# Kernel optimization log

Measured on AMD Instinct MI355X. Metric: run time of the kernel, lower is better.

## Reference

```python
import jax, jax.numpy as jnp
import numpy as np

N_NODES = 100000
N_EDGES = 1600000
N_MOVES = 200000
D = 256          # in_channels
H = 512          # hidden_dim

def setup_inputs() -> dict:
    key = jax.random.key(0)
    ks = jax.random.split(key, 6)
    node_embeddings = jax.random.normal(ks[0], (N_NODES, D), dtype=jnp.float32)
    edge_index = jax.random.randint(ks[1], (2, N_EDGES), 0, N_NODES, dtype=jnp.int64)
    move_edge_idxs = jax.random.randint(ks[2], (N_MOVES,), 0, N_EDGES, dtype=jnp.int64)
    # torch Linear weights: [out, in], scaled like kaiming-uniform-ish
    W1 = jax.random.normal(ks[3], (H, 2 * D), dtype=jnp.float32) * (1.0 / np.sqrt(2 * D))
    b1 = jnp.zeros((H,), dtype=jnp.float32)
    W2 = jax.random.normal(ks[4], (H // 2, H), dtype=jnp.float32) * (1.0 / np.sqrt(H))
    b2 = jnp.zeros((H // 2,), dtype=jnp.float32)
    W3 = jax.random.normal(ks[5], (1, H // 2), dtype=jnp.float32) * (1.0 / np.sqrt(H // 2))
    b3 = jnp.zeros((1,), dtype=jnp.float32)
    return {"node_embeddings": node_embeddings, "edge_index": edge_index,
            "move_edge_idxs": move_edge_idxs, "W1": W1, "b1": b1,
            "W2": W2, "b2": b2, "W3": W3, "b3": b3}

def reference(node_embeddings, edge_index, move_edge_idxs, W1, b1, W2, b2, W3, b3):
    # candidate_moves = edge_index[:, move_edge_idxs].T -> [n_moves, 2]
    src = edge_index[0, move_edge_idxs]          # [n_moves]
    tgt = edge_index[1, move_edge_idxs]          # [n_moves]
    emb_src = node_embeddings[src]               # [n_moves, D]
    emb_tgt = node_embeddings[tgt]               # [n_moves, D]
    x = jnp.concatenate([emb_src, emb_tgt], axis=-1)   # [n_moves, 2D]
    # 3-layer MLP (dropout is identity in eval mode)
    h = jax.nn.relu(x @ W1.T + b1)               # [n_moves, H]
    h = jax.nn.relu(h @ W2.T + b2)               # [n_moves, H//2]
    logits = (h @ W3.T + b3).squeeze(-1)         # [n_moves]
    return logits
```

## Files before the change

### kernel.cpp

```cpp
#include <hip/hip_runtime.h>
#include <hip/hip_bf16.h>

typedef __attribute__((ext_vector_type(4))) float f32x4;
typedef __attribute__((ext_vector_type(8))) short bfrag;
typedef __attribute__((ext_vector_type(4))) float facc;
typedef __attribute__((ext_vector_type(8))) ushort u16x8;

#define N_MOVES 200000
#define N_EDGES 1600000
#define DEMB 256
#define KD 512
#define H1D 512
#define H2D 256
#define MT 128
#define NTHREADS 1024

__device__ __forceinline__ ushort f2b(float f) {
  union { float f; unsigned u; } x; x.f = f;
  unsigned r = (x.u + 0x7fffu + ((x.u >> 16) & 1u)) >> 16;
  return (ushort)r;
}
__device__ __forceinline__ float b2f(ushort h) {
  union { unsigned u; float f; } x; x.u = ((unsigned)h) << 16;
  return x.f;
}

__global__ void convert_w(const float* __restrict__ W1, const float* __restrict__ W2,
                          ushort* __restrict__ Wb) {
  int i = (blockIdx.x * 256 + threadIdx.x) * 4;
  const int n1 = H1D * KD;
  if (i < n1) {
    f32x4 v = *(const f32x4*)(W1 + i);
    ushort4 h = { f2b(v.x), f2b(v.y), f2b(v.z), f2b(v.w) };
    *(ushort4*)(Wb + i) = h;
  } else {
    int j = i - n1;
    f32x4 v = *(const f32x4*)(W2 + j);
    ushort4 h = { f2b(v.x), f2b(v.y), f2b(v.z), f2b(v.w) };
    *(ushort4*)(Wb + n1 + j) = h;
  }
}

__global__ void convert_emb(const float* __restrict__ E, ushort* __restrict__ Eb) {
  int i = (blockIdx.x * 256 + threadIdx.x) * 8;
  f32x4 a = *(const f32x4*)(E + i);
  f32x4 b = *(const f32x4*)(E + i + 4);
  u16x8 h = { f2b(a.x), f2b(a.y), f2b(a.z), f2b(a.w),
              f2b(b.x), f2b(b.y), f2b(b.z), f2b(b.w) };
  *(u16x8*)(Eb + i) = h;
}

template<int EMBBF>
__global__ __launch_bounds__(NTHREADS, 4)
void fused_mlp(const float* __restrict__ emb,
               const ushort* __restrict__ embb,
               const int* __restrict__ edge_index,
               const int* __restrict__ move_idx,
               const ushort* __restrict__ W1b,
               const float* __restrict__ b1,
               const ushort* __restrict__ W2b,
               const float* __restrict__ b2,
               const float* __restrict__ W3,
               const float* __restrict__ b3,
               float* __restrict__ out)
{
  __shared__ ushort bufA[MT][KD];
  __shared__ int   s_src[MT], s_tgt[MT];
  __shared__ float sW3[H2D];

  const int tid  = threadIdx.x;
  const int lane = tid & 63;
  const int wave = tid >> 6;
  const int m0   = blockIdx.x * MT;

  if (tid < MT) {
    int mi = m0 + tid;
    if (mi >= N_MOVES) mi = N_MOVES - 1;
    int e = move_idx[mi];
    s_src[tid] = edge_index[e];
    s_tgt[tid] = edge_index[N_EDGES + e];
  }
  if (tid < H2D) sW3[tid] = W3[tid];
  __syncthreads();

  const int arow = lane & 15;
  const int akB  = (lane >> 4) << 4;
  const int nq   = (lane >> 4) << 2;

  const ushort* wp0 = W1b + (size_t)(((wave << 5) + arow) * KD) + (akB >> 1);
  const ushort* wp1 = wp0 + 16 * KD;

  bfrag bA[2], bB[2];
  bA[0] = *(const bfrag*)(wp0);      bA[1] = *(const bfrag*)(wp1);
  bB[0] = *(const bfrag*)(wp0 + 32); bB[1] = *(const bfrag*)(wp1 + 32);

  if (EMBBF) {
    #pragma unroll
    for (int it = 0; it < 8; ++it) {
      int row  = (wave << 3) + it;
      int gl   = lane ^ (row & 7);
      int node = (gl < 32) ? s_src[row] : s_tgt[row];
      const ushort* gp = embb + (size_t)node * DEMB + ((size_t)(gl & 31) << 3);
      __builtin_amdgcn_global_load_lds(
          (const __attribute__((address_space(1))) void*)gp,
          (__attribute__((address_space(3))) void*)(&bufA[row][0]),
          16, 0, 0);
    }
  } else {
    for (int u = tid; u < MT * 128; u += NTHREADS) {
      int row = u >> 7;
      int c4  = u & 127;
      const float* sp = (c4 < 64) ? (emb + (size_t)s_src[row] * DEMB + (c4 << 2))
                                  : (emb + (size_t)s_tgt[row] * DEMB + ((c4 - 64) << 2));
      f32x4 v = *(const f32x4*)sp;
      ushort4 h = { f2b(v.x), f2b(v.y), f2b(v.z), f2b(v.w) };
      int bo = (c4 << 3) ^ ((row & 7) << 4);
      *(ushort4*)((char*)(&bufA[row][0]) + bo) = h;
    }
  }
  __syncthreads();

  facc acc[8][2];
  #pragma unroll
  for (int mg = 0; mg < 8; ++mg) {
    acc[mg][0] = (facc){0.f, 0.f, 0.f, 0.f};
    acc[mg][1] = (facc){0.f, 0.f, 0.f, 0.f};
  }

  bfrag aE[8];
  #pragma unroll
  for (int mg = 0; mg < 8; ++mg) {
    int row = (mg << 4) + arow;
    int bo = akB ^ ((row & 7) << 4);
    aE[mg] = *(const bfrag*)((const char*)(&bufA[row][0]) + bo);
  }

  #pragma unroll
  for (int kk2 = 0; kk2 < 8; ++kk2) {
    const int kk = kk2 << 1;
    __builtin_amdgcn_s_setprio(1);
    #pragma unroll
    for (int mg = 0; mg < 8; ++mg) {
      acc[mg][0] = __builtin_amdgcn_mfma_f32_16x16x32_bf16(bA[0], aE[mg], acc[mg][0], 0, 0, 0);
      acc[mg][1] = __builtin_amdgcn_mfma_f32_16x16x32_bf16(bA[1], aE[mg], acc[mg][1], 0, 0, 0);
    }
    __builtin_amdgcn_s_setprio(0);
    #pragma unroll
    for (int mg = 0; mg < 8; ++mg) {
      int row = (mg << 4) + arow;
      int bo = (((kk + 1) << 6) + akB) ^ ((row & 7) << 4);
      aE[mg] = *(const bfrag*)((const char*)(&bufA[row][0]) + bo);
    }
    if (kk + 2 < 16) {
      bA[0] = *(const bfrag*)(wp0 + ((kk + 2) << 5));
      bA[1] = *(const bfrag*)(wp1 + ((kk + 2) << 5));
    }
    __builtin_amdgcn_s_setprio(1);
    #pragma unroll
    for (int mg = 0; mg < 8; ++mg) {
      acc[mg][0] = __builtin_amdgcn_mfma_f32_16x16x32_bf16(bB[0], aE[mg], acc[mg][0], 0, 0, 0);
      acc[mg][1] = __builtin_amdgcn_mfma_f32_16x16x32_bf16(bB[1], aE[mg], acc[mg][1], 0, 0, 0);
    }
    __builtin_amdgcn_s_setprio(0);
    if (kk2 < 7) {
      #pragma unroll
      for (int mg = 0; mg < 8; ++mg) {
        int row = (mg << 4) + arow;
        int bo = (((kk + 2) << 6) + akB) ^ ((row & 7) << 4);
        aE[mg] = *(const bfrag*)((const char*)(&bufA[row][0]) + bo);
      }
      if (kk + 3 < 16) {
        bB[0] = *(const bfrag*)(wp0 + ((kk + 3) << 5));
        bB[1] = *(const bfrag*)(wp1 + ((kk + 3) << 5));
      }
    }
  }

  const ushort* cp0 = W2b + (size_t)(((wave << 4) + arow) * KD) + (akB >> 1);
  bfrag cA = *(const bfrag*)(cp0);
  bfrag cB = *(const bfrag*)(cp0 + 32);
  f32x4 bv1[2];
  bv1[0] = *(const f32x4*)(b1 + (wave << 5) + nq);
  bv1[1] = *(const f32x4*)(b1 + (wave << 5) + 16 + nq);

  __syncthreads();

  #pragma unroll
  for (int mg = 0; mg < 8; ++mg) {
    int m = (mg << 4) + arow;
    #pragma unroll
    for (int ng = 0; ng < 2; ++ng) {
      int nb = (wave << 5) + (ng << 4) + nq;
      ushort4 h;
      h.x = f2b(fmaxf(acc[mg][ng][0] + bv1[ng][0], 0.f));
      h.y = f2b(fmaxf(acc[mg][ng][1] + bv1[ng][1], 0.f));
      h.z = f2b(fmaxf(acc[mg][ng][2] + bv1[ng][2], 0.f));
      h.w = f2b(fmaxf(acc[mg][ng][3] + bv1[ng][3], 0.f));
      int bo = (nb << 1) ^ ((m & 7) << 4);
      *(ushort4*)((char*)(&bufA[0][0]) + m * (KD * 2) + bo) = h;
    }
  }
  __syncthreads();

  facc acc2[8];
  #pragma unroll
  for (int mg = 0; mg < 8; ++mg) acc2[mg] = (facc){0.f, 0.f, 0.f, 0.f};

  #pragma unroll
  for (int mg = 0; mg < 8; ++mg) {
    int row = (mg << 4) + arow;
    int bo = akB ^ ((row & 7) << 4);
    aE[mg] = *(const bfrag*)((const char*)(&bufA[row][0]) + bo);
  }

  #pragma unroll
  for (int kk2 = 0; kk2 < 8; ++kk2) {
    const int kk = kk2 << 1;
    __builtin_amdgcn_s_setprio(1);
    #pragma unroll
    for (int mg = 0; mg < 8; ++mg)
      acc2[mg] = __builtin_amdgcn_mfma_f32_16x16x32_bf16(cA, aE[mg], acc2[mg], 0, 0, 0);
    __builtin_amdgcn_s_setprio(0);
    #pragma unroll
    for (int mg = 0; mg < 8; ++mg) {
      int row = (mg << 4) + arow;
      int bo = (((kk + 1) << 6) + akB) ^ ((row & 7) << 4);
      aE[mg] = *(const bfrag*)((const char*)(&bufA[row][0]) + bo);
    }
    if (kk + 2 < 16) cA = *(const bfrag*)(cp0 + ((kk + 2) << 5));
    __builtin_amdgcn_s_setprio(1);
    #pragma unroll
    for (int mg = 0; mg < 8; ++mg)
      acc2[mg] = __builtin_amdgcn_mfma_f32_16x16x32_bf16(cB, aE[mg], acc2[mg], 0, 0, 0);
    __builtin_amdgcn_s_setprio(0);
    if (kk2 < 7) {
      #pragma unroll
      for (int mg = 0; mg < 8; ++mg) {
        int row = (mg << 4) + arow;
        int bo = (((kk + 2) << 6) + akB) ^ ((row & 7) << 4);
        aE[mg] = *(const bfrag*)((const char*)(&bufA[row][0]) + bo);
      }
      if (kk + 3 < 16) cB = *(const bfrag*)(cp0 + ((kk + 3) << 5));
    }
  }

  f32x4 bv2 = *(const f32x4*)(b2 + (wave << 4) + nq);

  __syncthreads();

  ushort (*H2s)[H2D] = (ushort(*)[H2D])bufA;
  #pragma unroll
  for (int mg = 0; mg < 8; ++mg) {
    int m = (mg << 4) + arow;
    int nb = (wave << 4) + nq;
    ushort4 h;
    h.x = f2b(fmaxf(acc2[mg][0] + bv2[0], 0.f));
    h.y = f2b(fmaxf(acc2[mg][1] + bv2[1], 0.f));
    h.z = f2b(fmaxf(acc2[mg][2] + bv2[2], 0.f));
    h.w = f2b(fmaxf(acc2[mg][3] + bv2[3], 0.f));
    int bo = (nb << 1) ^ ((m & 7) << 4);
    *(ushort4*)((char*)(&H2s[0][0]) + m * (H2D * 2) + bo) = h;
  }
  __syncthreads();

  {
    const float b3v = b3[0];
    int row = tid >> 3;
    int oct = tid & 7;
    float sum = 0.f;
    #pragma unroll
    for (int j = 0; j < 4; ++j) {
      int kb = (oct << 6) + (j << 4);
      int bo = kb ^ ((row & 7) << 4);
      bfrag hv = *(const bfrag*)((const char*)(&H2s[row][0]) + bo);
      int k0 = (oct << 5) + (j << 3);
      #pragma unroll
      for (int e = 0; e < 8; ++e)
        sum += b2f((ushort)hv[e]) * sW3[k0 + e];
    }
    sum += __shfl_xor(sum, 1);
    sum += __shfl_xor(sum, 2);
    sum += __shfl_xor(sum, 4);
    if (oct == 0 && (m0 + row) < N_MOVES) out[m0 + row] = sum + b3v;
  }
}

extern "C" void kernel_launch(void* const* d_in, const int* in_sizes, int n_in,
                              void* d_out, int out_size, void* d_ws, size_t ws_size,
                              hipStream_t stream) {
  const float* emb        = (const float*)d_in[0];
  const int*   edge_index = (const int*)d_in[1];
  const int*   move_idx   = (const int*)d_in[2];
  const float* W1         = (const float*)d_in[3];
  const float* b1         = (const float*)d_in[4];
  const float* W2         = (const float*)d_in[5];
  const float* b2         = (const float*)d_in[6];
  const float* W3         = (const float*)d_in[7];
  const float* b3         = (const float*)d_in[8];
  float* out = (float*)d_out;

  ushort* Wb   = (ushort*)d_ws;
  ushort* Embb = Wb + (H1D * KD + H2D * KD);
  const size_t need = (size_t)(H1D * KD + H2D * KD + 100000 * DEMB) * 2;
  const int grid = (N_MOVES + MT - 1) / MT;

  convert_w<<<384, 256, 0, stream>>>(W1, W2, Wb);

  if (ws_size >= need) {
    convert_emb<<<12500, 256, 0, stream>>>(emb, Embb);
    fused_mlp<1><<<grid, NTHREADS, 0, stream>>>(
        emb, Embb, edge_index, move_idx,
        Wb, b1, Wb + H1D * KD, b2, W3, b3, out);
  } else {
    fused_mlp<0><<<grid, NTHREADS, 0, stream>>>(
        emb, Embb, edge_index, move_idx,
        Wb, b1, Wb + H1D * KD, b2, W3, b3, out);
  }
}
```

Baseline: 498.3 us.

## Halve block threads and double per-wave N tile in fused MLP

Reduces the block from 16 to 8 waves and doubles each wave's output-column tile in both GEMM layers (4 N-fragments in layer 1, 2 in layer 2), with the gather and final dot-product loops adjusted to match. Each A-fragment read from LDS now feeds twice as many MFMAs, cutting LDS read traffic and per-wave overhead. The cost is more accumulator registers (32 facc per wave in layer 1) and a lower occupancy target of 2 blocks per CU, which may reduce latency hiding for the gather.

```diff
diff --git a/kernel.cpp b/kernel.cpp
--- a/kernel.cpp
+++ b/kernel.cpp
@@ -13,7 +13,7 @@
 #define H1D 512
 #define H2D 256
 #define MT 128
-#define NTHREADS 1024
+#define NTHREADS 512
 
 __device__ __forceinline__ ushort f2b(float f) {
   union { float f; unsigned u; } x; x.f = f;
@@ -51,7 +51,7 @@
 }
 
 template<int EMBBF>
-__global__ __launch_bounds__(NTHREADS, 4)
+__global__ __launch_bounds__(NTHREADS, 2)
 void fused_mlp(const float* __restrict__ emb,
                const ushort* __restrict__ embb,
                const int* __restrict__ edge_index,
@@ -87,17 +87,21 @@
   const int akB  = (lane >> 4) << 4;
   const int nq   = (lane >> 4) << 2;
 
-  const ushort* wp0 = W1b + (size_t)(((wave << 5) + arow) * KD) + (akB >> 1);
+  const ushort* wp0 = W1b + (size_t)(((wave << 6) + arow) * KD) + (akB >> 1);
   const ushort* wp1 = wp0 + 16 * KD;
-
-  bfrag bA[2], bB[2];
+  const ushort* wp2 = wp0 + 32 * KD;
+  const ushort* wp3 = wp0 + 48 * KD;
+
+  bfrag bA[4], bB[4];
   bA[0] = *(const bfrag*)(wp0);      bA[1] = *(const bfrag*)(wp1);
+  bA[2] = *(const bfrag*)(wp2);      bA[3] = *(const bfrag*)(wp3);
   bB[0] = *(const bfrag*)(wp0 + 32); bB[1] = *(const bfrag*)(wp1 + 32);
+  bB[2] = *(const bfrag*)(wp2 + 32); bB[3] = *(const bfrag*)(wp3 + 32);
 
   if (EMBBF) {
     #pragma unroll
-    for (int it = 0; it < 8; ++it) {
-      int row  = (wave << 3) + it;
+    for (int it = 0; it < 16; ++it) {
+      int row  = (wave << 4) + it;
       int gl   = lane ^ (row & 7);
       int node = (gl < 32) ? s_src[row] : s_tgt[row];
       const ushort* gp = embb + (size_t)node * DEMB + ((size_t)(gl & 31) << 3);
@@ -120,12 +124,12 @@
   }
   __syncthreads();
 
-  facc acc[8][2];
-  #pragma unroll
-  for (int mg = 0; mg < 8; ++mg) {
-    acc[mg][0] = (facc){0.f, 0.f, 0.f, 0.f};
-    acc[mg][1] = (facc){0.f, 0.f, 0.f, 0.f};
-  }
+  facc acc[8][4];
+  #pragma unroll
+  for (int mg = 0; mg < 8; ++mg)
+    #pragma unroll
+    for (int ng = 0; ng < 4; ++ng)
+      acc[mg][ng] = (facc){0.f, 0.f, 0.f, 0.f};
 
   bfrag aE[8];
   #pragma unroll
@@ -140,10 +144,10 @@
     const int kk = kk2 << 1;
     __builtin_amdgcn_s_setprio(1);
     #pragma unroll
-    for (int mg = 0; mg < 8; ++mg) {
-      acc[mg][0] = __builtin_amdgcn_mfma_f32_16x16x32_bf16(bA[0], aE[mg], acc[mg][0], 0, 0, 0);
-      acc[mg][1] = __builtin_amdgcn_mfma_f32_16x16x32_bf16(bA[1], aE[mg], acc[mg][1], 0, 0, 0);
-    }
+    for (int mg = 0; mg < 8; ++mg)
+      #pragma unroll
+      for (int ng = 0; ng < 4; ++ng)
+        acc[mg][ng] = __builtin_amdgcn_mfma_f32_16x16x32_bf16(bA[ng], aE[mg], acc[mg][ng], 0, 0, 0);
     __builtin_amdgcn_s_setprio(0);
     #pragma unroll
     for (int mg = 0; mg < 8; ++mg) {
@@ -154,13 +158,15 @@
     if (kk + 2 < 16) {
       bA[0] = *(const bfrag*)(wp0 + ((kk + 2) << 5));
       bA[1] = *(const bfrag*)(wp1 + ((kk + 2) << 5));
+      bA[2] = *(const bfrag*)(wp2 + ((kk + 2) << 5));
+      bA[3] = *(const bfrag*)(wp3 + ((kk + 2) << 5));
     }
     __builtin_amdgcn_s_setprio(1);
     #pragma unroll
-    for (int mg = 0; mg < 8; ++mg) {
-      acc[mg][0] = __builtin_amdgcn_mfma_f32_16x16x32_bf16(bB[0], aE[mg], acc[mg][0], 0, 0, 0);
-      acc[mg][1] = __builtin_amdgcn_mfma_f32_16x16x32_bf16(bB[1], aE[mg], acc[mg][1], 0, 0, 0);
-    }
+    for (int mg = 0; mg < 8; ++mg)
+      #pragma unroll
+      for (int ng = 0; ng < 4; ++ng)
+        acc[mg][ng] = __builtin_amdgcn_mfma_f32_16x16x32_bf16(bB[ng], aE[mg], acc[mg][ng], 0, 0, 0);
     __builtin_amdgcn_s_setprio(0);
     if (kk2 < 7) {
       #pragma unroll
@@ -172,16 +178,21 @@
       if (kk + 3 < 16) {
         bB[0] = *(const bfrag*)(wp0 + ((kk + 3) << 5));
         bB[1] = *(const bfrag*)(wp1 + ((kk + 3) << 5));
+        bB[2] = *(const bfrag*)(wp2 + ((kk + 3) << 5));
+        bB[3] = *(const bfrag*)(wp3 + ((kk + 3) << 5));
       }
     }
   }
 
-  const ushort* cp0 = W2b + (size_t)(((wave << 4) + arow) * KD) + (akB >> 1);
-  bfrag cA = *(const bfrag*)(cp0);
-  bfrag cB = *(const bfrag*)(cp0 + 32);
-  f32x4 bv1[2];
-  bv1[0] = *(const f32x4*)(b1 + (wave << 5) + nq);
-  bv1[1] = *(const f32x4*)(b1 + (wave << 5) + 16 + nq);
+  const ushort* cp0 = W2b + (size_t)(((wave << 5) + arow) * KD) + (akB >> 1);
+  const ushort* cp1 = cp0 + 16 * KD;
+  bfrag cA[2], cB[2];
+  cA[0] = *(const bfrag*)(cp0);      cA[1] = *(const bfrag*)(cp1);
+  cB[0] = *(const bfrag*)(cp0 + 32); cB[1] = *(const bfrag*)(cp1 + 32);
+  f32x4 bv1[4];
+  #pragma unroll
+  for (int ng = 0; ng < 4; ++ng)
+    bv1[ng] = *(const f32x4*)(b1 + (wave << 6) + (ng << 4) + nq);
 
   __syncthreads();
 
@@ -189,8 +200,8 @@
   for (int mg = 0; mg < 8; ++mg) {
     int m = (mg << 4) + arow;
     #pragma unroll
-    for (int ng = 0; ng < 2; ++ng) {
-      int nb = (wave << 5) + (ng << 4) + nq;
+    for (int ng = 0; ng < 4; ++ng) {
+      int nb = (wave << 6) + (ng << 4) + nq;
       ushort4 h;
       h.x = f2b(fmaxf(acc[mg][ng][0] + bv1[ng][0], 0.f));
       h.y = f2b(fmaxf(acc[mg][ng][1] + bv1[ng][1], 0.f));
@@ -202,9 +213,12 @@
   }
   __syncthreads();
 
-  facc acc2[8];
-  #pragma unroll
-  for (int mg = 0; mg < 8; ++mg) acc2[mg] = (facc){0.f, 0.f, 0.f, 0.f};
+  facc acc2[8][2];
+  #pragma unroll
+  for (int mg = 0; mg < 8; ++mg) {
+    acc2[mg][0] = (facc){0.f, 0.f, 0.f, 0.f};
+    acc2[mg][1] = (facc){0.f, 0.f, 0.f, 0.f};
+  }
 
   #pragma unroll
   for (int mg = 0; mg < 8; ++mg) {
@@ -218,8 +232,10 @@
     const int kk = kk2 << 1;
     __builtin_amdgcn_s_setprio(1);
     #pragma unroll
-    for (int mg = 0; mg < 8; ++mg)
-      acc2[mg] = __builtin_amdgcn_mfma_f32_16x16x32_bf16(cA, aE[mg], acc2[mg], 0, 0, 0);
+    for (int mg = 0; mg < 8; ++mg) {
+      acc2[mg][0] = __builtin_amdgcn_mfma_f32_16x16x32_bf16(cA[0], aE[mg], acc2[mg][0], 0, 0, 0);
+      acc2[mg][1] = __builtin_amdgcn_mfma_f32_16x16x32_bf16(cA[1], aE[mg], acc2[mg][1], 0, 0, 0);
+    }
     __builtin_amdgcn_s_setprio(0);
     #pragma unroll
     for (int mg = 0; mg < 8; ++mg) {
@@ -227,11 +243,16 @@
       int bo = (((kk + 1) << 6) + akB) ^ ((row & 7) << 4);
       aE[mg] = *(const bfrag*)((const char*)(&bufA[row][0]) + bo);
     }
-    if (kk + 2 < 16) cA = *(const bfrag*)(cp0 + ((kk + 2) << 5));
+    if (kk + 2 < 16) {
+      cA[0] = *(const bfrag*)(cp0 + ((kk + 2) << 5));
+      cA[1] = *(const bfrag*)(cp1 + ((kk + 2) << 5));
+    }
     __builtin_amdgcn_s_setprio(1);
     #pragma unroll
-    for (int mg = 0; mg < 8; ++mg)
-      acc2[mg] = __builtin_amdgcn_mfma_f32_16x16x32_bf16(cB, aE[mg], acc2[mg], 0, 0, 0);
+    for (int mg = 0; mg < 8; ++mg) {
+      acc2[mg][0] = __builtin_amdgcn_mfma_f32_16x16x32_bf16(cB[0], aE[mg], acc2[mg][0], 0, 0, 0);
+      acc2[mg][1] = __builtin_amdgcn_mfma_f32_16x16x32_bf16(cB[1], aE[mg], acc2[mg][1], 0, 0, 0);
+    }
     __builtin_amdgcn_s_setprio(0);
     if (kk2 < 7) {
       #pragma unroll
@@ -240,11 +261,16 @@
         int bo = (((kk + 2) << 6) + akB) ^ ((row & 7) << 4);
         aE[mg] = *(const bfrag*)((const char*)(&bufA[row][0]) + bo);
       }
-      if (kk + 3 < 16) cB = *(const bfrag*)(cp0 + ((kk + 3) << 5));
-    }
-  }
-
-  f32x4 bv2 = *(const f32x4*)(b2 + (wave << 4) + nq);
+      if (kk + 3 < 16) {
+        cB[0] = *(const bfrag*)(cp0 + ((kk + 3) << 5));
+        cB[1] = *(const bfrag*)(cp1 + ((kk + 3) << 5));
+      }
+    }
+  }
+
+  f32x4 bv2[2];
+  bv2[0] = *(const f32x4*)(b2 + (wave << 5) + nq);
+  bv2[1] = *(const f32x4*)(b2 + (wave << 5) + 16 + nq);
 
   __syncthreads();
 
@@ -252,35 +278,37 @@
   #pragma unroll
   for (int mg = 0; mg < 8; ++mg) {
     int m = (mg << 4) + arow;
-    int nb = (wave << 4) + nq;
-    ushort4 h;
-    h.x = f2b(fmaxf(acc2[mg][0] + bv2[0], 0.f));
-    h.y = f2b(fmaxf(acc2[mg][1] + bv2[1], 0.f));
-    h.z = f2b(fmaxf(acc2[mg][2] + bv2[2], 0.f));
-    h.w = f2b(fmaxf(acc2[mg][3] + bv2[3], 0.f));
-    int bo = (nb << 1) ^ ((m & 7) << 4);
-    *(ushort4*)((char*)(&H2s[0][0]) + m * (H2D * 2) + bo) = h;
+    #pragma unroll
+    for (int ng = 0; ng < 2; ++ng) {
+      int nb = (wave << 5) + (ng << 4) + nq;
+      ushort4 h;
+      h.x = f2b(fmaxf(acc2[mg][ng][0] + bv2[ng][0], 0.f));
+      h.y = f2b(fmaxf(acc2[mg][ng][1] + bv2[ng][1], 0.f));
+      h.z = f2b(fmaxf(acc2[mg][ng][2] + bv2[ng][2], 0.f));
+      h.w = f2b(fmaxf(acc2[mg][ng][3] + bv2[ng][3], 0.f));
+      int bo = (nb << 1) ^ ((m & 7) << 4);
+      *(ushort4*)((char*)(&H2s[0][0]) + m * (H2D * 2) + bo) = h;
+    }
   }
   __syncthreads();
 
   {
     const float b3v = b3[0];
-    int row = tid >> 3;
-    int oct = tid & 7;
+    int row = tid >> 2;
+    int oct = tid & 3;
     float sum = 0.f;
     #pragma unroll
-    for (int j = 0; j < 4; ++j) {
-      int kb = (oct << 6) + (j << 4);
+    for (int j = 0; j < 8; ++j) {
+      int kb = (oct << 7) + (j << 4);
       int bo = kb ^ ((row & 7) << 4);
       bfrag hv = *(const bfrag*)((const char*)(&H2s[row][0]) + bo);
-      int k0 = (oct << 5) + (j << 3);
+      int k0 = (oct << 6) + (j << 3);
       #pragma unroll
       for (int e = 0; e < 8; ++e)
         sum += b2f((ushort)hv[e]) * sW3[k0 + e];
     }
     sum += __shfl_xor(sum, 1);
     sum += __shfl_xor(sum, 2);
-    sum += __shfl_xor(sum, 4);
     if (oct == 0 && (m0 + row) < N_MOVES) out[m0 + row] = sum + b3v;
   }
 }
```

New measurement: 457.3 us. 8.2% less time.
